# Kernel optimization log

Measured on AMD Instinct MI355X. Metric: run time of the kernel, lower is better.

## Reference

```python
import jax, jax.numpy as jnp
import numpy as np

NUM_HEADS = 16
HEAD_DIM = 64  # hidden_dim 1024 / 16 heads
COH_DIM = 8
MOT_RANK = 4


def _linear(x, W, b):
    # torch nn.Linear: y = x @ W.T + b
    return jnp.einsum('...i,oi->...o', x, W) + b


def setup_inputs() -> dict:
    key = jax.random.key(0)
    ks = jax.random.split(key, 17)
    d, c, m = HEAD_DIM, COH_DIM, MOT_RANK
    s = 1.0 / np.sqrt(d)
    sc = 1.0 / np.sqrt(c)
    sm = 1.0 / np.sqrt(m)
    inp = {
        'x': jax.random.normal(ks[0], (4, 2048, 1024), dtype=jnp.float32),
        'Wi': jax.random.uniform(ks[1], (d, d), jnp.float32, -s, s),
        'bi': jax.random.uniform(ks[2], (d,), jnp.float32, -s, s),
        'Wq': jax.random.uniform(ks[3], (d, d), jnp.float32, -s, s),
        'bq': jax.random.uniform(ks[4], (d,), jnp.float32, -s, s),
        'Wk': jax.random.uniform(ks[5], (d, d), jnp.float32, -s, s),
        'bk': jax.random.uniform(ks[6], (d,), jnp.float32, -s, s),
        'Wv': jax.random.uniform(ks[7], (d, d), jnp.float32, -s, s),
        'bv': jax.random.uniform(ks[8], (d,), jnp.float32, -s, s),
        'Wc': jax.random.uniform(ks[9], (c, d), jnp.float32, -s, s),
        'bc': jax.random.uniform(ks[10], (c,), jnp.float32, -s, s),
        'Wci': jax.random.uniform(ks[11], (d, c), jnp.float32, -sc, sc),
        'bci': jax.random.uniform(ks[12], (d,), jnp.float32, -sc, sc),
        'Wm': jax.random.uniform(ks[13], (m, d), jnp.float32, -s, s),
        'bm': jax.random.uniform(ks[14], (m,), jnp.float32, -s, s),
        'Wmi': jax.random.uniform(ks[15], (d, m), jnp.float32, -sm, sm),
        'bmi': jax.random.uniform(ks[16], (d,), jnp.float32, -sm, sm),
    }
    return inp


def reference(x, Wi, bi, Wq, bq, Wk, bk, Wv, bv, Wc, bc, Wci, bci, Wm, bm, Wmi, bmi):
    B, S, D = x.shape
    H, hd = NUM_HEADS, HEAD_DIM
    # split heads: [B, H, S, hd]
    xh = x.reshape(B, S, H, hd).transpose(0, 2, 1, 3)
    # resolution * load_factor = 1.0 scaling (identity here), then input projection
    h = _linear(xh, Wi, bi)
    q = _linear(h, Wq, bq)
    k = _linear(h, Wk, bk)
    v = _linear(h, Wv, bv)
    # scaled dot-product attention per head
    scores = jnp.einsum('bhqd,bhkd->bhqk', q, k) / jnp.sqrt(jnp.float32(hd))
    attn = jax.nn.softmax(scores, axis=-1)
    out = jnp.einsum('bhqk,bhkd->bhqd', attn, v)
    # cohomology round-trip projection
    out = _linear(_linear(out, Wc, bc), Wci, bci)
    # motive round-trip projection
    out = _linear(_linear(out, Wm, bm), Wmi, bmi)
    # merge heads back to [B, S, D]
    return out.transpose(0, 2, 1, 3).reshape(B, S, D)
```

## Files before the change

### kernel.cpp

```cpp
#include <hip/hip_runtime.h>


#define SEQ 2048
#define DM  1024
#define HD  64
#define QS  0.180336880111120429f
#define THR 8.0f

typedef short bf16x8 __attribute__((ext_vector_type(8)));
typedef unsigned short u16x8 __attribute__((ext_vector_type(8)));
typedef float f32x16 __attribute__((ext_vector_type(16)));

#define MFMA32 __builtin_amdgcn_mfma_f32_32x32x16_bf16

#if defined(__has_builtin)
#if __has_builtin(__builtin_amdgcn_exp2f)
#define EXP2(x) __builtin_amdgcn_exp2f(x)
#endif
#endif
#ifndef EXP2
#define EXP2(x) exp2f(x)
#endif

#define KG_OFF  12288
#define VG_OFF  (12288 + 8388608)
#define WS_NEED ((size_t)512 + 2ull * (12288 + 2ull * 8388608))

__device__ __forceinline__ unsigned short f2bf(float f) {
    unsigned int v = __float_as_uint(f);
    unsigned int r = v + 0x7FFFu + ((v >> 16) & 1u);
    return (unsigned short)(r >> 16);
}
__device__ __forceinline__ unsigned int pk2r(float a, float b) {
    return __builtin_amdgcn_perm(__float_as_uint(b) + 0x8000u,
                                 __float_as_uint(a) + 0x8000u, 0x07060302u);
}
__device__ __forceinline__ unsigned int pk2t(float a, float b) {
    return __builtin_amdgcn_perm(__float_as_uint(b), __float_as_uint(a), 0x07060302u);
}
__device__ __forceinline__ unsigned int cvtpk(float a, float b) {
    unsigned int r;
    asm("v_cvt_pk_bf16_f32 %0, %1, %2" : "=v"(r) : "v"(a), "v"(b));
    return r;
}
__device__ __forceinline__ void swap32(unsigned int& a, unsigned int& b) {
    asm("v_permlane32_swap_b32 %0, %1" : "+v"(a), "+v"(b));
}
__device__ __forceinline__ f32x16 z16() {
    f32x16 v;
    #pragma unroll
    for (int i = 0; i < 16; i++) v[i] = 0.f;
    return v;
}

__device__ __forceinline__ void pack2(const f32x16 s, bf16x8& fA, bf16x8& fB) {
    union { bf16x8 v; unsigned int u[4]; } a, b;
    a.u[0] = cvtpk(s[0], s[1]);   a.u[1] = cvtpk(s[2], s[3]);
    a.u[2] = cvtpk(s[4], s[5]);   a.u[3] = cvtpk(s[6], s[7]);
    b.u[0] = cvtpk(s[8], s[9]);   b.u[1] = cvtpk(s[10], s[11]);
    b.u[2] = cvtpk(s[12], s[13]); b.u[3] = cvtpk(s[14], s[15]);
    swap32(a.u[0], a.u[2]); swap32(a.u[1], a.u[3]);
    swap32(b.u[0], b.u[2]); swap32(b.u[1], b.u[3]);
    fA = a.v; fB = b.v;
}

__device__ __forceinline__ void mm16L(const float* __restrict__ wrow,
                                      const float* __restrict__ L, int i0,
                                      float* __restrict__ acc) {
    #pragma unroll
    for (int ii = 0; ii < 16; ii++) acc[ii] = 0.f;
    for (int t = 0; t < 64; t += 4) {
        float4 w4 = *(const float4*)(wrow + t);
        #pragma unroll
        for (int d = 0; d < 4; d++) {
            float wv = (d == 0) ? w4.x : (d == 1) ? w4.y : (d == 2) ? w4.z : w4.w;
            const float* lr = L + (t + d) * 68 + i0;
            float4 a = *(const float4*)lr;
            float4 b = *(const float4*)(lr + 4);
            float4 c = *(const float4*)(lr + 8);
            float4 e = *(const float4*)(lr + 12);
            acc[0] += wv * a.x;  acc[1] += wv * a.y;  acc[2]  += wv * a.z;  acc[3]  += wv * a.w;
            acc[4] += wv * b.x;  acc[5] += wv * b.y;  acc[6]  += wv * b.z;  acc[7]  += wv * b.w;
            acc[8] += wv * c.x;  acc[9] += wv * c.y;  acc[10] += wv * c.z;  acc[11] += wv * c.w;
            acc[12] += wv * e.x; acc[13] += wv * e.y; acc[14] += wv * e.z;  acc[15] += wv * e.w;
        }
    }
}

__global__ __launch_bounds__(256)
void qmt_combine(const float* __restrict__ Wi,  const float* __restrict__ bi,
                 const float* __restrict__ Wq,  const float* __restrict__ bq,
                 const float* __restrict__ Wk,  const float* __restrict__ bk,
                 const float* __restrict__ Wv,  const float* __restrict__ bv,
                 const float* __restrict__ Wc,  const float* __restrict__ bc,
                 const float* __restrict__ Wci, const float* __restrict__ bci,
                 const float* __restrict__ Wm,  const float* __restrict__ bm,
                 const float* __restrict__ Wmi, const float* __restrict__ bmi,
                 float* __restrict__ ws) {
    const int tid = threadIdx.x;
    const int o = tid & 63;
    const int i0 = (tid >> 6) * 16;
    const bool lead = (tid < 64);
    const int role = blockIdx.x;

    __shared__ float Wa_s[64 * 68];
    __shared__ float Wi_s[64 * 68];
    __shared__ float Wvi_s[64 * 68];
    __shared__ float M_s[64 * 68];
    __shared__ float Wc_s[512];
    __shared__ float Wci_s[512];
    __shared__ float Wm_s[256];
    __shared__ float Wmi_s[256];
    __shared__ float bi_s[64], bvi_s[64], c1[64], c2[4];
    __shared__ float U1[32], U2[256];

    unsigned short* wsu = (unsigned short*)(ws + 128);
    const float* Wa = (role == 0) ? Wq : (role == 1) ? Wk : Wv;

    for (int i4 = tid; i4 < 1024; i4 += 256) {
        int r = i4 >> 4, c = (i4 & 15) * 4;
        *(float4*)&Wi_s[r * 68 + c] = *(const float4*)(Wi + i4 * 4);
        *(float4*)&Wa_s[r * 68 + c] = *(const float4*)(Wa + i4 * 4);
    }
    if (role == 2) {
        if (tid < 128) {
            *(float4*)&Wc_s[tid * 4]  = *(const float4*)(Wc + tid * 4);
            *(float4*)&Wci_s[tid * 4] = *(const float4*)(Wci + tid * 4);
        } else if (tid < 192) {
            int t = tid - 128;
            *(float4*)&Wm_s[t * 4]  = *(const float4*)(Wm + t * 4);
            *(float4*)&Wmi_s[t * 4] = *(const float4*)(Wmi + t * 4);
        }
    }
    if (lead) bi_s[o] = bi[o];
    __syncthreads();

    float acc[16];
    if (role == 0) {
        mm16L(Wa_s + o * 68, Wi_s, i0, acc);
        #pragma unroll
        for (int ii = 0; ii < 16; ii++) wsu[o * 64 + i0 + ii] = f2bf(acc[ii] * QS);
        if (lead) {
            float s = bq[o];
            for (int t = 0; t < 64; t++) s += Wa_s[o * 68 + t] * bi_s[t];
            ws[o] = s * QS;
        }
        return;
    }
    if (role == 1) {
        mm16L(Wa_s + o * 68, Wi_s, i0, acc);
        #pragma unroll
        for (int ii = 0; ii < 16; ii++) wsu[4096 + o * 64 + i0 + ii] = f2bf(acc[ii]);
        return;
    }
    mm16L(Wa_s + o * 68, Wi_s, i0, acc);
    #pragma unroll
    for (int ii = 0; ii < 16; ii++) Wvi_s[o * 68 + i0 + ii] = acc[ii];
    if (lead) {
        float s = bv[o];
        for (int t = 0; t < 64; t++) s += Wa_s[o * 68 + t] * bi_s[t];
        bvi_s[o] = s;
    }
    if (tid < 32) {
        int a = tid >> 3, c = tid & 7;
        float s = 0.f;
        for (int t = 0; t < 64; t++) s += Wm_s[a * 64 + t] * Wci_s[t * 8 + c];
        U1[a * 8 + c] = s;
    }
    __syncthreads();
    if (lead) {
        for (int a = 0; a < 4; a++) {
            float s = 0.f;
            for (int cc = 0; cc < 8; cc++) s += U1[a * 8 + cc] * Wc_s[cc * 64 + o];
            U2[a * 64 + o] = s;
        }
        float s = bci[o];
        for (int j = 0; j < 8; j++) s += Wci_s[o * 8 + j] * bc[j];
        c1[o] = s;
    }
    __syncthreads();
    #pragma unroll
    for (int ii = 0; ii < 16; ii++) {
        float s = 0.f;
        for (int a = 0; a < 4; a++) s += Wmi_s[o * 4 + a] * U2[a * 64 + i0 + ii];
        M_s[o * 68 + i0 + ii] = s;
    }
    if (tid < 4) {
        float s = bm[tid];
        for (int i = 0; i < 64; i++) s += Wm_s[tid * 64 + i] * c1[i];
        c2[tid] = s;
    }
    __syncthreads();
    mm16L(M_s + o * 68, Wvi_s, i0, acc);
    #pragma unroll
    for (int ii = 0; ii < 16; ii++) wsu[8192 + o * 64 + i0 + ii] = f2bf(acc[ii]);
    if (lead) {
        float bvv = 0.f;
        for (int t = 0; t < 64; t++) bvv += M_s[o * 68 + t] * bvi_s[t];
        float cvv = bmi[o];
        for (int a = 0; a < 4; a++) cvv += Wmi_s[o * 4 + a] * c2[a];
        ws[64 + o] = cvv + bvv;
    }
}

__global__ __launch_bounds__(256)
void qmt_kv(const float* __restrict__ x, float* __restrict__ ws) {
    const int tid = threadIdx.x;
    const int w = tid >> 6;
    const int lane = tid & 63;
    const int ln = lane & 31;
    const int h = lane >> 5;
    const int b = blockIdx.y >> 4;
    const int hh = blockIdx.y & 15;
    const int kt = blockIdx.x;

    const unsigned short* wsu = (const unsigned short*)(ws + 128);
    unsigned short* Kg = (unsigned short*)(ws + 128) + KG_OFF + (size_t)blockIdx.y * (2048 * 64);
    unsigned short* Vg = (unsigned short*)(ws + 128) + VG_OFF + (size_t)blockIdx.y * (64 * 2048);

    const int krl = (w >> 1) * 32 + ln;
    const int dt32 = (w & 1) * 32;

    bf16x8 akf[4], avf[4];
    #pragma unroll
    for (int c = 0; c < 4; c++) {
        int row = dt32 + ln;
        int col = c * 16 + h * 8;
        akf[c] = *(const bf16x8*)(wsu + 4096 + row * 64 + col);
        avf[c] = *(const bf16x8*)(wsu + 8192 + row * 64 + col);
    }
    bf16x8 xf[4];
    const float* xr = x + ((size_t)(b * SEQ + kt * 64 + krl) * DM + hh * HD);
    #pragma unroll
    for (int c = 0; c < 4; c++) {
        const float* p = xr + c * 16 + h * 8;
        float4 f0 = *(const float4*)p;
        float4 f1 = *(const float4*)(p + 4);
        union { bf16x8 v; unsigned int u[4]; } tt;
        tt.u[0] = pk2t(f0.x, f0.y); tt.u[1] = pk2t(f0.z, f0.w);
        tt.u[2] = pk2t(f1.x, f1.y); tt.u[3] = pk2t(f1.z, f1.w);
        xf[c] = tt.v;
    }
    f32x16 kacc = z16(), vacc = z16();
    #pragma unroll
    for (int c = 0; c < 4; c++) kacc = MFMA32(akf[c], xf[c], kacc, 0, 0, 0);
    #pragma unroll
    for (int c = 0; c < 4; c++) vacc = MFMA32(xf[c], avf[c], vacc, 0, 0, 0);
    #pragma unroll
    for (int g = 0; g < 4; g++) {
        uint2 pk_, pv_;
        pk_.x = cvtpk(kacc[4 * g + 0], kacc[4 * g + 1]);
        pk_.y = cvtpk(kacc[4 * g + 2], kacc[4 * g + 3]);
        *(uint2*)&Kg[(size_t)(kt * 64 + krl) * 64 + dt32 + 8 * g + 4 * h] = pk_;
        pv_.x = cvtpk(vacc[4 * g + 0], vacc[4 * g + 1]);
        pv_.y = cvtpk(vacc[4 * g + 2], vacc[4 * g + 3]);
        *(uint2*)&Vg[(size_t)(dt32 + ln) * 2048 + kt * 64 + (w >> 1) * 32 + 8 * g + 4 * h] = pv_;
    }
}

__global__ __launch_bounds__(256, 4)
void qmt_attn2(const float* __restrict__ x, const float* __restrict__ wsf,
               float* __restrict__ out) {
    __shared__ __align__(16) unsigned short ks_s[64 * 64];
    __shared__ __align__(16) unsigned short vt_s[64 * 64];
    __shared__ float als_l[128];
    __shared__ float ls_l[128];

    const int tid = threadIdx.x;
    const int w = tid >> 6;
    const int lane = tid & 63;
    const int ln = lane & 31;
    const int h = lane >> 5;
    const int b = blockIdx.y >> 4;
    const int hh = blockIdx.y & 15;
    const int qbase = blockIdx.x * 128;

    const unsigned short* wsu = (const unsigned short*)(wsf + 128);
    const unsigned short* Kg = wsu + KG_OFF + (size_t)blockIdx.y * (2048 * 64);
    const unsigned short* Vg = wsu + VG_OFF + (size_t)blockIdx.y * (64 * 2048);

    const float ec0 = wsf[64 + ln];
    const float ec1 = wsf[96 + ln];

    const int srow = tid >> 3;
    const int scol = (tid & 7) * 8;
    const int sch = (((tid & 7) ^ (srow & 7)) * 8);
    const int swm = ln & 7;

    u16x8 ka = *(const u16x8*)(Kg + (size_t)srow * 64 + scol);
    u16x8 kb = *(const u16x8*)(Kg + (size_t)(srow + 32) * 64 + scol);
    u16x8 va = *(const u16x8*)(Vg + (size_t)srow * 2048 + scol);
    u16x8 vb = *(const u16x8*)(Vg + (size_t)(srow + 32) * 2048 + scol);

    bf16x8 qf[4];
    {
        bf16x8 xq[4];
        const float* xrow = x + ((size_t)(b * SEQ + qbase + w * 32 + ln) * DM + hh * HD);
        #pragma unroll
        for (int c = 0; c < 4; c++) {
            const float* p = xrow + c * 16 + h * 8;
            float4 f0 = *(const float4*)p;
            float4 f1 = *(const float4*)(p + 4);
            union { bf16x8 v; unsigned int u[4]; } t;
            t.u[0] = pk2t(f0.x, f0.y); t.u[1] = pk2t(f0.z, f0.w);
            t.u[2] = pk2t(f1.x, f1.y); t.u[3] = pk2t(f1.z, f1.w);
            xq[c] = t.v;
        }
        #pragma unroll
        for (int m = 0; m < 2; m++) {
            f32x16 acc;
            #pragma unroll
            for (int g = 0; g < 4; g++) {
                float4 b4 = *(const float4*)&wsf[m * 32 + 8 * g + 4 * h];
                acc[4 * g + 0] = b4.x; acc[4 * g + 1] = b4.y;
                acc[4 * g + 2] = b4.z; acc[4 * g + 3] = b4.w;
            }
            #pragma unroll
            for (int c = 0; c < 4; c++) {
                bf16x8 aq = *(const bf16x8*)(wsu + (m * 32 + ln) * 64 + c * 16 + h * 8);
                acc = MFMA32(aq, xq[c], acc, 0, 0, 0);
            }
            pack2(acc, qf[2 * m], qf[2 * m + 1]);
        }
    }

    f32x16 o0 = z16(), o1 = z16();
    float m_i = -1e30f, l_i = 0.f;

    *(u16x8*)&ks_s[srow * 64 + sch] = ka;
    *(u16x8*)&ks_s[(srow + 32) * 64 + sch] = kb;
    *(u16x8*)&vt_s[srow * 64 + sch] = va;
    *(u16x8*)&vt_s[(srow + 32) * 64 + sch] = vb;
    __syncthreads();

    for (int kt = 0; kt < SEQ / 64; kt++) {
        const bool more = (kt < SEQ / 64 - 1);
        if (more) {
            const int kn = (kt + 1) * 64;
            ka = *(const u16x8*)(Kg + (size_t)(kn + srow) * 64 + scol);
            kb = *(const u16x8*)(Kg + (size_t)(kn + srow + 32) * 64 + scol);
            va = *(const u16x8*)(Vg + (size_t)srow * 2048 + kn + scol);
            vb = *(const u16x8*)(Vg + (size_t)(srow + 32) * 2048 + kn + scol);
        }

        f32x16 st0 = z16(), st1 = z16();
        #pragma unroll
        for (int c = 0; c < 4; c++) {
            const int ci = ((c * 2 + h) ^ swm) * 8;
            bf16x8 k0 = *(const bf16x8*)&ks_s[ln * 64 + ci];
            bf16x8 k1 = *(const bf16x8*)&ks_s[(32 + ln) * 64 + ci];
            st0 = MFMA32(k0, qf[c], st0, 0, 0, 0);
            st1 = MFMA32(k1, qf[c], st1, 0, 0, 0);
        }

        float tm[8];
        #pragma unroll
        for (int i = 0; i < 8; i++)
            tm[i] = fmaxf(fmaxf(st0[i], st0[i + 8]), fmaxf(st1[i], st1[i + 8]));
        #pragma unroll
        for (int i = 0; i < 4; i++) tm[i] = fmaxf(tm[i], tm[i + 4]);
        float mx = fmaxf(fmaxf(tm[0], tm[1]), fmaxf(tm[2], tm[3]));
        mx = fmaxf(mx, __shfl_xor(mx, 32));

        const bool need = __any(mx > m_i + THR) != 0;
        float mn = m_i, al = 1.0f;
        if (need) {
            mn = fmaxf(m_i, mx);
            al = EXP2(m_i - mn);
            if (lane < 32) als_l[w * 32 + lane] = al;
        }

        #pragma unroll
        for (int i = 0; i < 16; i++) st0[i] = EXP2(st0[i] - mn);
        #pragma unroll
        for (int i = 0; i < 16; i++) st1[i] = EXP2(st1[i] - mn);
        float sm[8];
        #pragma unroll
        for (int i = 0; i < 8; i++)
            sm[i] = (st0[i] + st0[i + 8]) + (st1[i] + st1[i + 8]);
        #pragma unroll
        for (int i = 0; i < 4; i++) sm[i] += sm[i + 4];
        float ss = (sm[0] + sm[1]) + (sm[2] + sm[3]);
        ss += __shfl_xor(ss, 32);
        l_i = l_i * al + ss;
        m_i = mn;

        bf16x8 pf[4];
        pack2(st0, pf[0], pf[1]);
        pack2(st1, pf[2], pf[3]);

        if (need) {
            #pragma unroll
            for (int g = 0; g < 4; g++) {
                float4 a4 = *(const float4*)&als_l[w * 32 + 8 * g + 4 * h];
                o0[4 * g + 0] *= a4.x; o0[4 * g + 1] *= a4.y;
                o0[4 * g + 2] *= a4.z; o0[4 * g + 3] *= a4.w;
                o1[4 * g + 0] *= a4.x; o1[4 * g + 1] *= a4.y;
                o1[4 * g + 2] *= a4.z; o1[4 * g + 3] *= a4.w;
            }
        }

        #pragma unroll
        for (int c = 0; c < 4; c++) {
            const int ci = ((c * 2 + h) ^ swm) * 8;
            bf16x8 v0 = *(const bf16x8*)&vt_s[ln * 64 + ci];
            bf16x8 v1 = *(const bf16x8*)&vt_s[(32 + ln) * 64 + ci];
            o0 = MFMA32(pf[c], v0, o0, 0, 0, 0);
            o1 = MFMA32(pf[c], v1, o1, 0, 0, 0);
        }
        __syncthreads();
        if (more) {
            *(u16x8*)&ks_s[srow * 64 + sch] = ka;
            *(u16x8*)&ks_s[(srow + 32) * 64 + sch] = kb;
            *(u16x8*)&vt_s[srow * 64 + sch] = va;
            *(u16x8*)&vt_s[(srow + 32) * 64 + sch] = vb;
        }
        __syncthreads();
    }

    if (lane < 32) ls_l[w * 32 + lane] = l_i;
    #pragma unroll
    for (int g = 0; g < 4; g++) {
        float4 l4 = *(const float4*)&ls_l[w * 32 + 8 * g + 4 * h];
        float4 iv = make_float4(1.f / l4.x, 1.f / l4.y, 1.f / l4.z, 1.f / l4.w);
        #pragma unroll
        for (int i = 0; i < 4; i++) {
            float ivv = (i == 0) ? iv.x : (i == 1) ? iv.y : (i == 2) ? iv.z : iv.w;
            int q = qbase + w * 32 + 8 * g + 4 * h + i;
            float* orow = out + ((size_t)(b * SEQ + q) * DM + hh * HD);
            orow[ln] = o0[4 * g + i] * ivv + ec0;
            orow[32 + ln] = o1[4 * g + i] * ivv + ec1;
        }
    }
}

__global__ __launch_bounds__(256, 3)
void qmt_attn_fb(const float* __restrict__ x, const float* __restrict__ wsf,
                 float* __restrict__ out) {
    __shared__ __align__(16) unsigned short ps_s[128 * 72];
    __shared__ __align__(16) unsigned short ks_s[64 * 72];
    __shared__ __align__(16) unsigned short vt_s[64 * 72];
    __shared__ float als_l[128];
    __shared__ float ls_l[128];

    const int tid = threadIdx.x;
    const int w = tid >> 6;
    const int lane = tid & 63;
    const int ln = lane & 31;
    const int h = lane >> 5;
    const int b = blockIdx.y >> 4;
    const int hh = blockIdx.y & 15;
    const int qbase = blockIdx.x * 128;

    const unsigned short* wsu = (const unsigned short*)(wsf + 128);

    bf16x8 akf[4], avf[4];
    #pragma unroll
    for (int c = 0; c < 4; c++) {
        int row = (w & 1) * 32 + ln;
        int col = c * 16 + h * 8;
        akf[c] = *(const bf16x8*)(wsu + 4096 + row * 64 + col);
        avf[c] = *(const bf16x8*)(wsu + 8192 + row * 64 + col);
    }
    const float ec0 = wsf[64 + ln];
    const float ec1 = wsf[96 + ln];

    bf16x8 qf[4];
    {
        bf16x8 xq[4];
        const float* xrow = x + ((size_t)(b * SEQ + qbase + w * 32 + ln) * DM + hh * HD);
        #pragma unroll
        for (int c = 0; c < 4; c++) {
            const float* p = xrow + c * 16 + h * 8;
            float4 f0 = *(const float4*)p;
            float4 f1 = *(const float4*)(p + 4);
            union { bf16x8 v; unsigned int u[4]; } t;
            t.u[0] = pk2t(f0.x, f0.y); t.u[1] = pk2t(f0.z, f0.w);
            t.u[2] = pk2t(f1.x, f1.y); t.u[3] = pk2t(f1.z, f1.w);
            xq[c] = t.v;
        }
        #pragma unroll
        for (int m = 0; m < 2; m++) {
            f32x16 acc;
            #pragma unroll
            for (int g = 0; g < 4; g++) {
                float4 b4 = *(const float4*)&wsf[m * 32 + 8 * g + 4 * h];
                acc[4 * g + 0] = b4.x; acc[4 * g + 1] = b4.y;
                acc[4 * g + 2] = b4.z; acc[4 * g + 3] = b4.w;
            }
            #pragma unroll
            for (int c = 0; c < 4; c++) {
                bf16x8 aq = *(const bf16x8*)(wsu + (m * 32 + ln) * 64 + c * 16 + h * 8);
                acc = MFMA32(aq, xq[c], acc, 0, 0, 0);
            }
            #pragma unroll
            for (int g = 0; g < 4; g++) {
                uint2 pw;
                pw.x = pk2r(acc[4 * g + 0], acc[4 * g + 1]);
                pw.y = pk2r(acc[4 * g + 2], acc[4 * g + 3]);
                *(uint2*)&ps_s[(w * 32 + ln) * 72 + m * 32 + 8 * g + 4 * h] = pw;
            }
        }
        #pragma unroll
        for (int c = 0; c < 4; c++)
            qf[c] = *(const bf16x8*)&ps_s[(w * 32 + ln) * 72 + c * 16 + h * 8];
    }

    f32x16 o0 = z16(), o1 = z16();
    float m_i = -1e30f, l_i = 0.f;

    const int krl = (w >> 1) * 32 + ln;
    const int dt32 = (w & 1) * 32;

    for (int kt = 0; kt < SEQ / 64; kt++) {
        bf16x8 xf[4];
        const float* xr = x + ((size_t)(b * SEQ + kt * 64 + krl) * DM + hh * HD);
        #pragma unroll
        for (int c = 0; c < 4; c++) {
            const float* p = xr + c * 16 + h * 8;
            float4 f0 = *(const float4*)p;
            float4 f1 = *(const float4*)(p + 4);
            union { bf16x8 v; unsigned int u[4]; } t;
            t.u[0] = pk2t(f0.x, f0.y); t.u[1] = pk2t(f0.z, f0.w);
            t.u[2] = pk2t(f1.x, f1.y); t.u[3] = pk2t(f1.z, f1.w);
            xf[c] = t.v;
        }
        f32x16 kacc = z16(), vacc = z16();
        #pragma unroll
        for (int c = 0; c < 4; c++) kacc = MFMA32(akf[c], xf[c], kacc, 0, 0, 0);
        #pragma unroll
        for (int c = 0; c < 4; c++) vacc = MFMA32(xf[c], avf[c], vacc, 0, 0, 0);
        #pragma unroll
        for (int g = 0; g < 4; g++) {
            uint2 pk_, pv_;
            pk_.x = pk2r(kacc[4 * g + 0], kacc[4 * g + 1]);
            pk_.y = pk2r(kacc[4 * g + 2], kacc[4 * g + 3]);
            *(uint2*)&ks_s[krl * 72 + dt32 + 8 * g + 4 * h] = pk_;
            pv_.x = pk2r(vacc[4 * g + 0], vacc[4 * g + 1]);
            pv_.y = pk2r(vacc[4 * g + 2], vacc[4 * g + 3]);
            *(uint2*)&vt_s[(dt32 + ln) * 72 + (w >> 1) * 32 + 8 * g + 4 * h] = pv_;
        }
        __syncthreads();

        f32x16 st0 = z16(), st1 = z16();
        #pragma unroll
        for (int c = 0; c < 4; c++) {
            bf16x8 k0 = *(const bf16x8*)&ks_s[ln * 72 + c * 16 + h * 8];
            bf16x8 k1 = *(const bf16x8*)&ks_s[(32 + ln) * 72 + c * 16 + h * 8];
            st0 = MFMA32(k0, qf[c], st0, 0, 0, 0);
            st1 = MFMA32(k1, qf[c], st1, 0, 0, 0);
        }
        float mx = st0[0];
        #pragma unroll
        for (int i = 1; i < 16; i++) mx = fmaxf(mx, st0[i]);
        #pragma unroll
        for (int i = 0; i < 16; i++) mx = fmaxf(mx, st1[i]);
        mx = fmaxf(mx, __shfl_xor(mx, 32));
        const float mn = fmaxf(m_i, mx);
        const float al = EXP2(m_i - mn);
        float ss = 0.f;
        #pragma unroll
        for (int i = 0; i < 16; i++) { st0[i] = EXP2(st0[i] - mn); ss += st0[i]; }
        #pragma unroll
        for (int i = 0; i < 16; i++) { st1[i] = EXP2(st1[i] - mn); ss += st1[i]; }
        ss += __shfl_xor(ss, 32);
        l_i = l_i * al + ss;
        m_i = mn;
        if (lane < 32) als_l[w * 32 + lane] = al;
        #pragma unroll
        for (int g = 0; g < 4; g++) {
            uint2 p0, p1;
            p0.x = pk2r(st0[4 * g + 0], st0[4 * g + 1]);
            p0.y = pk2r(st0[4 * g + 2], st0[4 * g + 3]);
            *(uint2*)&ps_s[(w * 32 + ln) * 72 + 8 * g + 4 * h] = p0;
            p1.x = pk2r(st1[4 * g + 0], st1[4 * g + 1]);
            p1.y = pk2r(st1[4 * g + 2], st1[4 * g + 3]);
            *(uint2*)&ps_s[(w * 32 + ln) * 72 + 32 + 8 * g + 4 * h] = p1;
        }
        #pragma unroll
        for (int g = 0; g < 4; g++) {
            float4 a4 = *(const float4*)&als_l[w * 32 + 8 * g + 4 * h];
            o0[4 * g + 0] *= a4.x; o0[4 * g + 1] *= a4.y;
            o0[4 * g + 2] *= a4.z; o0[4 * g + 3] *= a4.w;
            o1[4 * g + 0] *= a4.x; o1[4 * g + 1] *= a4.y;
            o1[4 * g + 2] *= a4.z; o1[4 * g + 3] *= a4.w;
        }
        #pragma unroll
        for (int c = 0; c < 4; c++) {
            bf16x8 pf = *(const bf16x8*)&ps_s[(w * 32 + ln) * 72 + c * 16 + h * 8];
            bf16x8 v0 = *(const bf16x8*)&vt_s[ln * 72 + c * 16 + h * 8];
            bf16x8 v1 = *(const bf16x8*)&vt_s[(32 + ln) * 72 + c * 16 + h * 8];
            o0 = MFMA32(pf, v0, o0, 0, 0, 0);
            o1 = MFMA32(pf, v1, o1, 0, 0, 0);
        }
        __syncthreads();
    }

    if (lane < 32) ls_l[w * 32 + lane] = l_i;
    #pragma unroll
    for (int g = 0; g < 4; g++) {
        float4 l4 = *(const float4*)&ls_l[w * 32 + 8 * g + 4 * h];
        float4 iv = make_float4(1.f / l4.x, 1.f / l4.y, 1.f / l4.z, 1.f / l4.w);
        #pragma unroll
        for (int i = 0; i < 4; i++) {
            float ivv = (i == 0) ? iv.x : (i == 1) ? iv.y : (i == 2) ? iv.z : iv.w;
            int q = qbase + w * 32 + 8 * g + 4 * h + i;
            float* orow = out + ((size_t)(b * SEQ + q) * DM + hh * HD);
            orow[ln] = o0[4 * g + i] * ivv + ec0;
            orow[32 + ln] = o1[4 * g + i] * ivv + ec1;
        }
    }
}

extern "C" void kernel_launch(void* const* d_in, const int* in_sizes, int n_in,
                              void* d_out, int out_size, void* d_ws, size_t ws_size,
                              hipStream_t stream) {
    const float* x = (const float*)d_in[0];
    float* wsf = (float*)d_ws;

    qmt_combine<<<3, 256, 0, stream>>>(
        (const float*)d_in[1],  (const float*)d_in[2],
        (const float*)d_in[3],  (const float*)d_in[4],
        (const float*)d_in[5],  (const float*)d_in[6],
        (const float*)d_in[7],  (const float*)d_in[8],
        (const float*)d_in[9],  (const float*)d_in[10],
        (const float*)d_in[11], (const float*)d_in[12],
        (const float*)d_in[13], (const float*)d_in[14],
        (const float*)d_in[15], (const float*)d_in[16],
        wsf);

    if (ws_size >= WS_NEED) {
        dim3 gkv(SEQ / 64, 64);
        qmt_kv<<<gkv, 256, 0, stream>>>(x, wsf);
        dim3 grid(SEQ / 128, 64);
        qmt_attn2<<<grid, 256, 0, stream>>>(x, wsf, (float*)d_out);
    } else {
        dim3 grid(SEQ / 128, 64);
        qmt_attn_fb<<<grid, 256, 0, stream>>>(x, wsf, (float*)d_out);
    }
}
```

Measured before the change: 243.1 us.

## Double-buffer K/V LDS tiles with tile-contiguous global layout and XCD-aware block mapping

```diff
diff --git a/kernel.cpp b/kernel.cpp
--- a/kernel.cpp
+++ b/kernel.cpp
@@ -246,23 +246,27 @@
     for (int c = 0; c < 4; c++) kacc = MFMA32(akf[c], xf[c], kacc, 0, 0, 0);
     #pragma unroll
     for (int c = 0; c < 4; c++) vacc = MFMA32(xf[c], avf[c], vacc, 0, 0, 0);
+
+    unsigned short* KgT = Kg + kt * 4096;
+    unsigned short* VgT = Vg + kt * 4096;
     #pragma unroll
     for (int g = 0; g < 4; g++) {
+        const int idx = (((w * 4 + g) * 64) + 2 * ln + h) * 4;
         uint2 pk_, pv_;
         pk_.x = cvtpk(kacc[4 * g + 0], kacc[4 * g + 1]);
         pk_.y = cvtpk(kacc[4 * g + 2], kacc[4 * g + 3]);
-        *(uint2*)&Kg[(size_t)(kt * 64 + krl) * 64 + dt32 + 8 * g + 4 * h] = pk_;
+        *(uint2*)&KgT[idx] = pk_;
         pv_.x = cvtpk(vacc[4 * g + 0], vacc[4 * g + 1]);
         pv_.y = cvtpk(vacc[4 * g + 2], vacc[4 * g + 3]);
-        *(uint2*)&Vg[(size_t)(dt32 + ln) * 2048 + kt * 64 + (w >> 1) * 32 + 8 * g + 4 * h] = pv_;
+        *(uint2*)&VgT[idx] = pv_;
     }
 }
 
 __global__ __launch_bounds__(256, 4)
 void qmt_attn2(const float* __restrict__ x, const float* __restrict__ wsf,
                float* __restrict__ out) {
-    __shared__ __align__(16) unsigned short ks_s[64 * 64];
-    __shared__ __align__(16) unsigned short vt_s[64 * 64];
+    __shared__ __align__(16) unsigned short ks_s[2][64 * 72];
+    __shared__ __align__(16) unsigned short vt_s[2][64 * 72];
     __shared__ float als_l[128];
     __shared__ float ls_l[128];
 
@@ -271,26 +275,45 @@
     const int lane = tid & 63;
     const int ln = lane & 31;
     const int h = lane >> 5;
-    const int b = blockIdx.y >> 4;
-    const int hh = blockIdx.y & 15;
-    const int qbase = blockIdx.x * 128;
+    const int bid = blockIdx.x;
+    const int wg = (bid & 7) * 128 + (bid >> 3);
+    const int bh = wg >> 4;
+    const int qbase = (wg & 15) * 128;
+    const int b = bh >> 4;
+    const int hh = bh & 15;
 
     const unsigned short* wsu = (const unsigned short*)(wsf + 128);
-    const unsigned short* Kg = wsu + KG_OFF + (size_t)blockIdx.y * (2048 * 64);
-    const unsigned short* Vg = wsu + VG_OFF + (size_t)blockIdx.y * (64 * 2048);
+    const unsigned short* Kg = wsu + KG_OFF + (size_t)bh * (2048 * 64);
+    const unsigned short* Vg = wsu + VG_OFF + (size_t)bh * (64 * 2048);
 
     const float ec0 = wsf[64 + ln];
     const float ec1 = wsf[96 + ln];
 
-    const int srow = tid >> 3;
-    const int scol = (tid & 7) * 8;
-    const int sch = (((tid & 7) ^ (srow & 7)) * 8);
-    const int swm = ln & 7;
-
-    u16x8 ka = *(const u16x8*)(Kg + (size_t)srow * 64 + scol);
-    u16x8 kb = *(const u16x8*)(Kg + (size_t)(srow + 32) * 64 + scol);
-    u16x8 va = *(const u16x8*)(Vg + (size_t)srow * 2048 + scol);
-    u16x8 vb = *(const u16x8*)(Vg + (size_t)(srow + 32) * 2048 + scol);
+    const int r1 = tid >> 5, p1 = tid & 31, r2 = r1 + 8;
+    const int ldsK1 = (((r1 >> 3) & 1) * 32 + p1) * 72 + ((r1 >> 2) & 1) * 32 + (r1 & 3) * 8;
+    const int ldsK2 = (((r2 >> 3) & 1) * 32 + p1) * 72 + ((r2 >> 2) & 1) * 32 + (r2 & 3) * 8;
+    const int ldsV1 = (((r1 >> 2) & 1) * 32 + p1) * 72 + ((r1 >> 3) & 1) * 32 + (r1 & 3) * 8;
+    const int ldsV2 = (((r2 >> 2) & 1) * 32 + p1) * 72 + ((r2 >> 3) & 1) * 32 + (r2 & 3) * 8;
+    const int gk1 = tid * 8;
+    const int gk2 = 2048 + tid * 8;
+
+    u16x8 ka, kb, va, vb;
+    auto loadT = [&](int kt_) {
+        const unsigned short* Kt = Kg + kt_ * 4096;
+        const unsigned short* Vt = Vg + kt_ * 4096;
+        ka = *(const u16x8*)(Kt + gk1);
+        kb = *(const u16x8*)(Kt + gk2);
+        va = *(const u16x8*)(Vt + gk1);
+        vb = *(const u16x8*)(Vt + gk2);
+    };
+    auto storeT = [&](int bb) {
+        *(u16x8*)&ks_s[bb][ldsK1] = ka;
+        *(u16x8*)&ks_s[bb][ldsK2] = kb;
+        *(u16x8*)&vt_s[bb][ldsV1] = va;
+        *(u16x8*)&vt_s[bb][ldsV2] = vb;
+    };
+
+    loadT(0);
 
     bf16x8 qf[4];
     {
@@ -327,31 +350,28 @@
     f32x16 o0 = z16(), o1 = z16();
     float m_i = -1e30f, l_i = 0.f;
 
-    *(u16x8*)&ks_s[srow * 64 + sch] = ka;
-    *(u16x8*)&ks_s[(srow + 32) * 64 + sch] = kb;
-    *(u16x8*)&vt_s[srow * 64 + sch] = va;
-    *(u16x8*)&vt_s[(srow + 32) * 64 + sch] = vb;
+    storeT(0);
+    loadT(1);
     __syncthreads();
 
     for (int kt = 0; kt < SEQ / 64; kt++) {
-        const bool more = (kt < SEQ / 64 - 1);
-        if (more) {
-            const int kn = (kt + 1) * 64;
-            ka = *(const u16x8*)(Kg + (size_t)(kn + srow) * 64 + scol);
-            kb = *(const u16x8*)(Kg + (size_t)(kn + srow + 32) * 64 + scol);
-            va = *(const u16x8*)(Vg + (size_t)srow * 2048 + kn + scol);
-            vb = *(const u16x8*)(Vg + (size_t)(srow + 32) * 2048 + kn + scol);
-        }
+        const int cur = kt & 1;
+        if (kt + 1 < SEQ / 64) storeT(cur ^ 1);
+        if (kt + 2 < SEQ / 64) loadT(kt + 2);
+
+        const unsigned short* ks = ks_s[cur];
+        const unsigned short* vt = vt_s[cur];
 
         f32x16 st0 = z16(), st1 = z16();
+        __builtin_amdgcn_s_setprio(1);
         #pragma unroll
         for (int c = 0; c < 4; c++) {
-            const int ci = ((c * 2 + h) ^ swm) * 8;
-            bf16x8 k0 = *(const bf16x8*)&ks_s[ln * 64 + ci];
-            bf16x8 k1 = *(const bf16x8*)&ks_s[(32 + ln) * 64 + ci];
+            bf16x8 k0 = *(const bf16x8*)&ks[ln * 72 + c * 16 + h * 8];
+            bf16x8 k1 = *(const bf16x8*)&ks[(32 + ln) * 72 + c * 16 + h * 8];
             st0 = MFMA32(k0, qf[c], st0, 0, 0, 0);
             st1 = MFMA32(k1, qf[c], st1, 0, 0, 0);
         }
+        __builtin_amdgcn_s_setprio(0);
 
         float tm[8];
         #pragma unroll
@@ -400,21 +420,16 @@
             }
         }
 
+        __builtin_amdgcn_s_setprio(1);
         #pragma unroll
         for (int c = 0; c < 4; c++) {
-            const int ci = ((c * 2 + h) ^ swm) * 8;
-            bf16x8 v0 = *(const bf16x8*)&vt_s[ln * 64 + ci];
-            bf16x8 v1 = *(const bf16x8*)&vt_s[(32 + ln) * 64 + ci];
+            bf16x8 v0 = *(const bf16x8*)&vt[ln * 72 + c * 16 + h * 8];
+            bf16x8 v1 = *(const bf16x8*)&vt[(32 + ln) * 72 + c * 16 + h * 8];
             o0 = MFMA32(pf[c], v0, o0, 0, 0, 0);
             o1 = MFMA32(pf[c], v1, o1, 0, 0, 0);
         }
-        __syncthreads();
-        if (more) {
-            *(u16x8*)&ks_s[srow * 64 + sch] = ka;
-            *(u16x8*)&ks_s[(srow + 32) * 64 + sch] = kb;
-            *(u16x8*)&vt_s[srow * 64 + sch] = va;
-            *(u16x8*)&vt_s[(srow + 32) * 64 + sch] = vb;
-        }
+        __builtin_amdgcn_s_setprio(0);
+
         __syncthreads();
     }
 
@@ -632,8 +647,7 @@
     if (ws_size >= WS_NEED) {
         dim3 gkv(SEQ / 64, 64);
         qmt_kv<<<gkv, 256, 0, stream>>>(x, wsf);
-        dim3 grid(SEQ / 128, 64);
-        qmt_attn2<<<grid, 256, 0, stream>>>(x, wsf, (float*)d_out);
+        qmt_attn2<<<1024, 256, 0, stream>>>(x, wsf, (float*)d_out);
     } else {
         dim3 grid(SEQ / 128, 64);
         qmt_attn_fb<<<grid, 256, 0, stream>>>(x, wsf, (float*)d_out);
```

Measured after the change: 228.0 us. -6.2%, faster.
